# Optimization experiments

Hardware: AMD Instinct MI355X
Metric: run time of the kernel (lower is better)

Reference implementation:

```python
import jax, jax.numpy as jnp
import numpy as np

DIM = 1024
NUM_HEADS = 16
HEAD_DIM = DIM // NUM_HEADS
SCALE = HEAD_DIM ** -0.5


def setup_inputs() -> dict:
    key = jax.random.key(0)
    ks = jax.random.split(key, 9)
    s = 0.02
    return {
        "x": jax.random.normal(ks[0], (4, 2048, DIM), dtype=jnp.float32),
        "Wq": jax.random.normal(ks[1], (DIM, DIM), dtype=jnp.float32) * s,
        "bq": jax.random.normal(ks[2], (DIM,), dtype=jnp.float32) * s,
        "Wk": jax.random.normal(ks[3], (DIM, DIM), dtype=jnp.float32) * s,
        "bk": jax.random.normal(ks[4], (DIM,), dtype=jnp.float32) * s,
        "Wv": jax.random.normal(ks[5], (DIM, DIM), dtype=jnp.float32) * s,
        "bv": jax.random.normal(ks[6], (DIM,), dtype=jnp.float32) * s,
        "Wo": jax.random.normal(ks[7], (DIM, DIM), dtype=jnp.float32) * s,
        "bo": jax.random.normal(ks[8], (DIM,), dtype=jnp.float32) * s,
    }


def reference(x, Wq, bq, Wk, bk, Wv, bv, Wo, bo):
    B, S, D = x.shape
    H, Dh = NUM_HEADS, HEAD_DIM

    def heads(t):  # [B,S,D] -> [B,H,S,Dh]
        return t.reshape(B, S, H, Dh).transpose(0, 2, 1, 3)

    q = heads(x @ Wq.T + bq)
    k = heads(x @ Wk.T + bk)
    v = heads(x @ Wv.T + bv)

    attn = jnp.einsum('bnqd,bnkd->bnqk', q, k) * SCALE
    attn = jax.nn.softmax(attn, axis=-1)
    out = jnp.einsum('bnqk,bnkd->bnqd', attn, v)  # [B,H,S,Dh]
    out = out.transpose(0, 2, 1, 3).reshape(B, S, D)
    return out @ Wo.T + bo
```

## Files before the change

### kernel.cpp

```cpp
#include <hip/hip_runtime.h>
#include <stdint.h>

#define DIMD 1024
#define NH   16
#define DH   64
#define BB   4
#define SS   2048
#define MTOT 8192

static constexpr float QSCALE = 0.18033688011112042f;

typedef unsigned short u16;
typedef __attribute__((ext_vector_type(8))) short bf8;
typedef __attribute__((ext_vector_type(4))) float f4;
typedef __attribute__((ext_vector_type(16))) float f16v;

#if __has_builtin(__builtin_amdgcn_exp2f)
#define EXP2(x) __builtin_amdgcn_exp2f(x)
#else
#define EXP2(x) exp2f(x)
#endif

__device__ inline u16 f2bf(float f) {
    union { float f; uint32_t u; } v; v.f = f;
    uint32_t r = v.u + 0x7fffu + ((v.u >> 16) & 1u);
    return (u16)(r >> 16);
}

__device__ inline void gld16(const void* g, void* l) {
    __builtin_amdgcn_global_load_lds(
        (const __attribute__((address_space(1))) uint32_t*)g,
        (__attribute__((address_space(3))) uint32_t*)l, 16, 0, 0);
}

__device__ inline uint32_t cvtpk(float lo, float hi) {
    uint32_t r;
    asm("v_cvt_pk_bf16_f32 %0, %1, %2" : "=v"(r) : "v"(lo), "v"(hi));
    return r;
}

__global__ void cvt_all(const float* __restrict__ x,
                        const float* __restrict__ Wq, const float* __restrict__ Wk,
                        const float* __restrict__ Wv, const float* __restrict__ Wo,
                        u16* __restrict__ xb, u16* __restrict__ Wb)
{
    const int blk = blockIdx.x;
    const float* src;
    u16* dst;
    size_t base;
    if (blk < 8192) {
        src = x; dst = xb; base = (size_t)blk * 1024;
    } else {
        int wi = (blk - 8192) >> 10;
        src = (wi == 0) ? Wq : (wi == 1) ? Wk : (wi == 2) ? Wv : Wo;
        dst = Wb + (size_t)wi * DIMD * DIMD;
        base = (size_t)((blk - 8192) & 1023) * 1024;
    }
    size_t i = base + threadIdx.x * 4;
    float4 v = *(const float4*)(src + i);
    ushort4 o;
    o.x = f2bf(v.x); o.y = f2bf(v.y); o.z = f2bf(v.z); o.w = f2bf(v.w);
    *(ushort4*)(dst + i) = o;
}

__global__ __launch_bounds__(256, 2) void gemm_qkv(
    const u16* __restrict__ xb, const u16* __restrict__ Wb,
    const float* __restrict__ bq, const float* __restrict__ bk, const float* __restrict__ bv,
    u16* __restrict__ qkv, u16* __restrict__ vtb)
{
    __shared__ u16 lA[128 * 64];
    __shared__ u16 lB[128 * 64];
    const int tid = threadIdx.x;
    const int bm = blockIdx.x, bn = blockIdx.y, z = blockIdx.z;
    const u16* W = Wb + (size_t)z * DIMD * DIMD;
    const float* bias = (z == 0) ? bq : ((z == 1) ? bk : bv);
    u16* outp = qkv + (size_t)z * (size_t)MTOT * DIMD;

    const int lane = tid & 63, w = tid >> 6;
    const int wr = (w >> 1) * 64, wc = (w & 1) * 64;
    f4 acc[4][4] = {};

    const char* Abase = (const char*)xb + (size_t)(bm * 128) * 2048;
    const char* Bbase = (const char*)W + (size_t)(bn * 128) * 2048;

    for (int kt = 0; kt < 16; ++kt) {
        __syncthreads();
        #pragma unroll
        for (int p = 0; p < 4; ++p) {
            int off = (p * 256 + tid) * 16;
            int row = off >> 7, cb = off & 127;
            int scb = cb ^ ((row & 7) << 4);
            gld16(Abase + (size_t)row * 2048 + kt * 128 + scb, (char*)lA + off);
            gld16(Bbase + (size_t)row * 2048 + kt * 128 + scb, (char*)lB + off);
        }
        __syncthreads();
        #pragma unroll
        for (int ks = 0; ks < 2; ++ks) {
            const int cb = ks * 64 + ((lane >> 4) << 4);
            bf8 af[4], bfr[4];
            #pragma unroll
            for (int mi = 0; mi < 4; ++mi) {
                int r = wr + mi * 16 + (lane & 15);
                af[mi] = *(const bf8*)((const char*)lA + r * 128 + (cb ^ ((r & 7) << 4)));
            }
            #pragma unroll
            for (int ni = 0; ni < 4; ++ni) {
                int r = wc + ni * 16 + (lane & 15);
                bfr[ni] = *(const bf8*)((const char*)lB + r * 128 + (cb ^ ((r & 7) << 4)));
            }
            #pragma unroll
            for (int mi = 0; mi < 4; ++mi)
                #pragma unroll
                for (int ni = 0; ni < 4; ++ni)
                    acc[mi][ni] = __builtin_amdgcn_mfma_f32_16x16x32_bf16(af[mi], bfr[ni], acc[mi][ni], 0, 0, 0);
        }
    }

    if (z == 2) {
        #pragma unroll
        for (int ni = 0; ni < 4; ++ni) {
            int col = bn * 128 + wc + ni * 16 + (lane & 15);
            float bi = bias[col];
            int h = col >> 6, dh = col & 63;
            #pragma unroll
            for (int mi = 0; mi < 4; ++mi) {
                int row0 = bm * 128 + wr + mi * 16 + ((lane >> 4) << 2);
                int b = row0 >> 11, s = row0 & 2047;
                ushort4 st;
                st.x = f2bf(acc[mi][ni][0] + bi);
                st.y = f2bf(acc[mi][ni][1] + bi);
                st.z = f2bf(acc[mi][ni][2] + bi);
                st.w = f2bf(acc[mi][ni][3] + bi);
                *(ushort4*)(vtb + ((size_t)(b * NH + h) * DH + dh) * SS + s) = st;
            }
        }
    } else {
        const float mulv = (z == 0) ? QSCALE : 1.0f;
        #pragma unroll
        for (int ni = 0; ni < 4; ++ni) {
            int col = bn * 128 + wc + ni * 16 + (lane & 15);
            float bi = bias[col];
            int h = col >> 6, dh = col & 63;
            #pragma unroll
            for (int mi = 0; mi < 4; ++mi) {
                #pragma unroll
                for (int r = 0; r < 4; ++r) {
                    int row = bm * 128 + wr + mi * 16 + ((lane >> 4) << 2) + r;
                    int b = row >> 11, s = row & 2047;
                    outp[(((size_t)(b * NH + h) * SS + s) << 6) + dh] = f2bf((acc[mi][ni][r] + bi) * mulv);
                }
            }
        }
    }
}

__global__ __launch_bounds__(256, 2) void gemm_out(
    const u16* __restrict__ Ab, const u16* __restrict__ Wo,
    const float* __restrict__ bo, float* __restrict__ dout)
{
    __shared__ u16 lA[128 * 64];
    __shared__ u16 lB[128 * 64];
    const int tid = threadIdx.x;
    const int bm = blockIdx.x, bn = blockIdx.y;
    const int lane = tid & 63, w = tid >> 6;
    const int wr = (w >> 1) * 64, wc = (w & 1) * 64;
    f4 acc[4][4] = {};
    const char* Abase = (const char*)Ab + (size_t)(bm * 128) * 2048;
    const char* Bbase = (const char*)Wo + (size_t)(bn * 128) * 2048;

    for (int kt = 0; kt < 16; ++kt) {
        __syncthreads();
        #pragma unroll
        for (int p = 0; p < 4; ++p) {
            int off = (p * 256 + tid) * 16;
            int row = off >> 7, cb = off & 127;
            int scb = cb ^ ((row & 7) << 4);
            gld16(Abase + (size_t)row * 2048 + kt * 128 + scb, (char*)lA + off);
            gld16(Bbase + (size_t)row * 2048 + kt * 128 + scb, (char*)lB + off);
        }
        __syncthreads();
        #pragma unroll
        for (int ks = 0; ks < 2; ++ks) {
            const int cb = ks * 64 + ((lane >> 4) << 4);
            bf8 af[4], bfr[4];
            #pragma unroll
            for (int mi = 0; mi < 4; ++mi) {
                int r = wr + mi * 16 + (lane & 15);
                af[mi] = *(const bf8*)((const char*)lA + r * 128 + (cb ^ ((r & 7) << 4)));
            }
            #pragma unroll
            for (int ni = 0; ni < 4; ++ni) {
                int r = wc + ni * 16 + (lane & 15);
                bfr[ni] = *(const bf8*)((const char*)lB + r * 128 + (cb ^ ((r & 7) << 4)));
            }
            #pragma unroll
            for (int mi = 0; mi < 4; ++mi)
                #pragma unroll
                for (int ni = 0; ni < 4; ++ni)
                    acc[mi][ni] = __builtin_amdgcn_mfma_f32_16x16x32_bf16(af[mi], bfr[ni], acc[mi][ni], 0, 0, 0);
        }
    }
    #pragma unroll
    for (int ni = 0; ni < 4; ++ni) {
        int col = bn * 128 + wc + ni * 16 + (lane & 15);
        float bi = bo[col];
        #pragma unroll
        for (int mi = 0; mi < 4; ++mi) {
            #pragma unroll
            for (int r = 0; r < 4; ++r) {
                int row = bm * 128 + wr + mi * 16 + ((lane >> 4) << 2) + r;
                dout[(size_t)row * DIMD + col] = acc[mi][ni][r] + bi;
            }
        }
    }
}

__global__ __launch_bounds__(512, 4) void attn_fwd(
    const u16* __restrict__ Q, const u16* __restrict__ K,
    const u16* __restrict__ Vt, u16* __restrict__ O)
{
    __shared__ __align__(16) u16 lK[2][64 * 64];
    __shared__ __align__(16) u16 lV[3][64 * 64];

    const int tid = threadIdx.x;
    const int lane = tid & 63, w = tid >> 6;
    const int hi = lane >> 5, l31 = lane & 31;
    const int bh = blockIdx.y;
    const int qb0 = blockIdx.x * 256;
    const char* Kbase = (const char*)(K + (size_t)bh * SS * DH);
    const char* Vbase = (const char*)(Vt + (size_t)bh * DH * SS);

    const int qrow = qb0 + w * 32 + l31;
    const u16* Qp = Q + (size_t)bh * SS * DH + (size_t)qrow * DH;
    bf8 qf[4];
    #pragma unroll
    for (int kd = 0; kd < 4; ++kd)
        qf[kd] = *(const bf8*)(Qp + kd * 16 + hi * 8);

    f16v oacc0 = {}, oacc1 = {};
    float lsum = 0.f;
    bf8 pbv[4];

    const int rswz = (l31 & 7) << 4;

    auto stage = [&](int t, int vbuf) {
        int off = tid * 16;
        int row = off >> 7, cb = off & 127;
        int scb = cb ^ ((row & 7) << 4);
        int kv0 = t * 64;
        gld16(Kbase + (size_t)(kv0 + row) * 128 + scb, (char*)lK[t & 1] + off);
        gld16(Vbase + (size_t)row * (SS * 2) + (size_t)kv0 * 2 + scb, (char*)lV[vbuf] + off);
    };

    auto QKfn = [&](const char* lKc, f16v& s0, f16v& s1) {
        __builtin_amdgcn_s_setprio(1);
        #pragma unroll
        for (int kd = 0; kd < 4; ++kd) {
            const int colb = 32 * kd + 16 * hi;
            bf8 kf0 = *(const bf8*)(lKc + l31 * 128 + (colb ^ rswz));
            bf8 kf1 = *(const bf8*)(lKc + (32 + l31) * 128 + (colb ^ rswz));
            s0 = __builtin_amdgcn_mfma_f32_32x32x16_bf16(kf0, qf[kd], s0, 0, 0, 0);
            s1 = __builtin_amdgcn_mfma_f32_32x32x16_bf16(kf1, qf[kd], s1, 0, 0, 0);
        }
        __builtin_amdgcn_s_setprio(0);
    };

    auto PVfn = [&](const char* lVc) {
        __builtin_amdgcn_s_setprio(1);
        #pragma unroll
        for (int ks = 0; ks < 4; ++ks) {
            const int colb = 32 * ks + 16 * hi;
            bf8 vf0 = *(const bf8*)(lVc + l31 * 128 + (colb ^ rswz));
            bf8 vf1 = *(const bf8*)(lVc + (32 + l31) * 128 + (colb ^ rswz));
            oacc0 = __builtin_amdgcn_mfma_f32_32x32x16_bf16(vf0, pbv[ks], oacc0, 0, 0, 0);
            oacc1 = __builtin_amdgcn_mfma_f32_32x32x16_bf16(vf1, pbv[ks], oacc1, 0, 0, 0);
        }
        __builtin_amdgcn_s_setprio(0);
    };

    auto SMfn = [&](f16v& s0, f16v& s1) {
        float ps[16];
        #pragma unroll
        for (int i = 0; i < 16; ++i) {
            float e0 = EXP2(s0[i]);
            float e1 = EXP2(s1[i]);
            s0[i] = e0; s1[i] = e1;
            ps[i] = e0 + e1;
        }
        float t0 = (ps[0] + ps[1]) + (ps[2] + ps[3]);
        float t1 = (ps[4] + ps[5]) + (ps[6] + ps[7]);
        float t2 = (ps[8] + ps[9]) + (ps[10] + ps[11]);
        float t3 = (ps[12] + ps[13]) + (ps[14] + ps[15]);
        lsum += (t0 + t1) + (t2 + t3);

        uint32_t wv0[8], wv1[8];
        #pragma unroll
        for (int a = 0; a < 4; ++a) {
            wv0[a * 2 + 0] = cvtpk(s0[4 * a + 0], s0[4 * a + 1]);
            wv0[a * 2 + 1] = cvtpk(s0[4 * a + 2], s0[4 * a + 3]);
            wv1[a * 2 + 0] = cvtpk(s1[4 * a + 0], s1[4 * a + 1]);
            wv1[a * 2 + 1] = cvtpk(s1[4 * a + 2], s1[4 * a + 3]);
        }
        #pragma unroll
        for (int ks = 0; ks < 4; ++ks) {
            const int kss = ks & 1;
            uint32_t w0 = (ks < 2) ? wv0[4 * kss + 0] : wv1[4 * kss + 0];
            uint32_t w1 = (ks < 2) ? wv0[4 * kss + 1] : wv1[4 * kss + 1];
            uint32_t w2 = (ks < 2) ? wv0[4 * kss + 2] : wv1[4 * kss + 2];
            uint32_t w3 = (ks < 2) ? wv0[4 * kss + 3] : wv1[4 * kss + 3];
            asm("v_permlane32_swap_b32 %0, %1" : "+v"(w0), "+v"(w2));
            asm("v_permlane32_swap_b32 %0, %1" : "+v"(w1), "+v"(w3));
            union { uint32_t u[4]; bf8 v; } pb;
            pb.u[0] = w0; pb.u[1] = w1; pb.u[2] = w2; pb.u[3] = w3;
            pbv[ks] = pb.v;
        }
    };

    stage(0, 0);
    __syncthreads();
    {
        stage(1, 1);
        f16v s0 = {}, s1 = {};
        QKfn((const char*)lK[0], s0, s1);
        SMfn(s0, s1);
        __syncthreads();
    }

    int vW = 2;
    int vR = 0;
    for (int t = 1; t < SS / 64; ++t) {
        if (t + 1 < SS / 64) stage(t + 1, vW);
        f16v s0 = {}, s1 = {};
        QKfn((const char*)lK[t & 1], s0, s1);
        PVfn((const char*)lV[vR]);
        SMfn(s0, s1);
        __syncthreads();
        vW = (vW == 2) ? 0 : vW + 1;
        vR = (vR == 2) ? 0 : vR + 1;
    }
    PVfn((const char*)lV[vR]);

    const float l = lsum + __shfl_xor(lsum, 32, 64);
    const int b = bh >> 4, h = bh & 15;
    const float inv = 1.f / l;
    u16* orow = O + (((size_t)(b * SS + qrow)) << 10) + h * DH;
    #pragma unroll
    for (int g = 0; g < 4; ++g) {
        ushort4 st0, st1;
        st0.x = f2bf(oacc0[4 * g + 0] * inv); st0.y = f2bf(oacc0[4 * g + 1] * inv);
        st0.z = f2bf(oacc0[4 * g + 2] * inv); st0.w = f2bf(oacc0[4 * g + 3] * inv);
        st1.x = f2bf(oacc1[4 * g + 0] * inv); st1.y = f2bf(oacc1[4 * g + 1] * inv);
        st1.z = f2bf(oacc1[4 * g + 2] * inv); st1.w = f2bf(oacc1[4 * g + 3] * inv);
        *(ushort4*)(orow + 8 * g + 4 * hi) = st0;
        *(ushort4*)(orow + 32 + 8 * g + 4 * hi) = st1;
    }
}

extern "C" void kernel_launch(void* const* d_in, const int* in_sizes, int n_in,
                              void* d_out, int out_size, void* d_ws, size_t ws_size,
                              hipStream_t stream) {
    const float* x  = (const float*)d_in[0];
    const float* Wq = (const float*)d_in[1];
    const float* bq = (const float*)d_in[2];
    const float* Wk = (const float*)d_in[3];
    const float* bk = (const float*)d_in[4];
    const float* Wv = (const float*)d_in[5];
    const float* bv = (const float*)d_in[6];
    const float* Wo = (const float*)d_in[7];
    const float* bo = (const float*)d_in[8];
    float* out = (float*)d_out;

    u16* wsp = (u16*)d_ws;
    const size_t NX = (size_t)MTOT * DIMD;
    const size_t NW = (size_t)DIMD * DIMD;
    u16* xb   = wsp;
    u16* Wb   = wsp + NX;
    u16* Qb   = wsp + NX + 4 * NW;
    u16* Kb   = Qb + NX;
    u16* Vtb  = Kb + NX;
    u16* attn = xb;

    cvt_all<<<dim3(12288), 256, 0, stream>>>(x, Wq, Wk, Wv, Wo, xb, Wb);

    gemm_qkv<<<dim3(MTOT / 128, DIMD / 128, 3), 256, 0, stream>>>(xb, Wb, bq, bk, bv, Qb, Vtb);
    attn_fwd<<<dim3(SS / 256, BB * NH), 512, 0, stream>>>(Qb, Kb, Vtb, attn);
    gemm_out<<<dim3(MTOT / 128, DIMD / 128), 256, 0, stream>>>(attn, Wb + 3 * NW, bo, out);
}
```

Baseline: 174.2 us.

## Load V fragments directly from global into registers instead of LDS staging

Removes the triple-buffered LDS staging of V tiles in the attention kernel. Each lane now loads its V^T MFMA operands straight from global memory into registers one tile ahead, issued after the PV MFMAs behind a scheduling barrier. This cuts LDS traffic and LDS footprint. In exchange it adds register pressure (launch bounds relaxed from 4 to 2 waves/SIMD) and makes the PV step depend on global-load latency being hidden by the softmax and the next QK.

```diff
diff --git a/kernel.cpp b/kernel.cpp
--- a/kernel.cpp
+++ b/kernel.cpp
@@ -215,12 +215,11 @@
     }
 }
 
-__global__ __launch_bounds__(512, 4) void attn_fwd(
+__global__ __launch_bounds__(512, 2) void attn_fwd(
     const u16* __restrict__ Q, const u16* __restrict__ K,
     const u16* __restrict__ Vt, u16* __restrict__ O)
 {
     __shared__ __align__(16) u16 lK[2][64 * 64];
-    __shared__ __align__(16) u16 lV[3][64 * 64];
 
     const int tid = threadIdx.x;
     const int lane = tid & 63, w = tid >> 6;
@@ -240,16 +239,27 @@
     f16v oacc0 = {}, oacc1 = {};
     float lsum = 0.f;
     bf8 pbv[4];
+    bf8 vr[8];
 
     const int rswz = (l31 & 7) << 4;
 
-    auto stage = [&](int t, int vbuf) {
+    const char* vp0 = Vbase + (size_t)l31 * (SS * 2) + 16 * hi;
+    const char* vp1 = Vbase + (size_t)(32 + l31) * (SS * 2) + 16 * hi;
+
+    auto vload = [&](int t) {
+        const char* p0 = vp0 + t * 128;
+        const char* p1 = vp1 + t * 128;
+        vr[0] = *(const bf8*)(p0 + 0);  vr[1] = *(const bf8*)(p1 + 0);
+        vr[2] = *(const bf8*)(p0 + 32); vr[3] = *(const bf8*)(p1 + 32);
+        vr[4] = *(const bf8*)(p0 + 64); vr[5] = *(const bf8*)(p1 + 64);
+        vr[6] = *(const bf8*)(p0 + 96); vr[7] = *(const bf8*)(p1 + 96);
+    };
+
+    auto stageK = [&](int t) {
         int off = tid * 16;
         int row = off >> 7, cb = off & 127;
         int scb = cb ^ ((row & 7) << 4);
-        int kv0 = t * 64;
-        gld16(Kbase + (size_t)(kv0 + row) * 128 + scb, (char*)lK[t & 1] + off);
-        gld16(Vbase + (size_t)row * (SS * 2) + (size_t)kv0 * 2 + scb, (char*)lV[vbuf] + off);
+        gld16(Kbase + (size_t)(t * 64 + row) * 128 + scb, (char*)lK[t & 1] + off);
     };
 
     auto QKfn = [&](const char* lKc, f16v& s0, f16v& s1) {
@@ -265,15 +275,12 @@
         __builtin_amdgcn_s_setprio(0);
     };
 
-    auto PVfn = [&](const char* lVc) {
+    auto PVfn = [&]() {
         __builtin_amdgcn_s_setprio(1);
         #pragma unroll
         for (int ks = 0; ks < 4; ++ks) {
-            const int colb = 32 * ks + 16 * hi;
-            bf8 vf0 = *(const bf8*)(lVc + l31 * 128 + (colb ^ rswz));
-            bf8 vf1 = *(const bf8*)(lVc + (32 + l31) * 128 + (colb ^ rswz));
-            oacc0 = __builtin_amdgcn_mfma_f32_32x32x16_bf16(vf0, pbv[ks], oacc0, 0, 0, 0);
-            oacc1 = __builtin_amdgcn_mfma_f32_32x32x16_bf16(vf1, pbv[ks], oacc1, 0, 0, 0);
+            oacc0 = __builtin_amdgcn_mfma_f32_32x32x16_bf16(vr[2 * ks + 0], pbv[ks], oacc0, 0, 0, 0);
+            oacc1 = __builtin_amdgcn_mfma_f32_32x32x16_bf16(vr[2 * ks + 1], pbv[ks], oacc1, 0, 0, 0);
         }
         __builtin_amdgcn_s_setprio(0);
     };
@@ -316,29 +323,28 @@
         }
     };
 
-    stage(0, 0);
+    stageK(0);
+    vload(0);
     __syncthreads();
     {
-        stage(1, 1);
+        stageK(1);
         f16v s0 = {}, s1 = {};
         QKfn((const char*)lK[0], s0, s1);
         SMfn(s0, s1);
         __syncthreads();
     }
 
-    int vW = 2;
-    int vR = 0;
     for (int t = 1; t < SS / 64; ++t) {
-        if (t + 1 < SS / 64) stage(t + 1, vW);
+        if (t + 1 < SS / 64) stageK(t + 1);
         f16v s0 = {}, s1 = {};
         QKfn((const char*)lK[t & 1], s0, s1);
-        PVfn((const char*)lV[vR]);
+        PVfn();
+        __builtin_amdgcn_sched_barrier(0);
+        vload(t);
         SMfn(s0, s1);
         __syncthreads();
-        vW = (vW == 2) ? 0 : vW + 1;
-        vR = (vR == 2) ? 0 : vR + 1;
-    }
-    PVfn((const char*)lV[vR]);
+    }
+    PVfn();
 
     const float l = lsum + __shfl_xor(lsum, 32, 64);
     const int b = bh >> 4, h = bh & 15;
```

After: 272.4 us. 56.4% more time.
